# Kernel tuning notes

Hardware: AMD Instinct MI355X
Metric: run time of the kernel (lower is better)

## Reference

```python
import jax, jax.numpy as jnp
import numpy as np
from jax import lax

MAXHD = 200.0
MAXV = 40.0
MINA = -6.0
MAXA = 4.0
DT = 0.1
PAST = 25
NVEH = 4096
NT = 256


def setup_inputs() -> dict:
    key = jax.random.key(0)
    ks = jax.random.split(key, 8)
    s = 0.1
    return dict(
        lead_states=jax.random.uniform(ks[0], (NVEH, NT + PAST - 1, 2), dtype=jnp.float32),
        cur_states=jax.random.uniform(ks[1], (NVEH, PAST, 2), dtype=jnp.float32),
        mask=jnp.ones((NVEH, NT + PAST - 1), dtype=jnp.float32),
        conv1_w=jax.random.normal(ks[2], (3, 3, 32), dtype=jnp.float32) * s,
        conv1_b=jnp.zeros((32,), dtype=jnp.float32),
        conv2_w=jax.random.normal(ks[3], (3, 32, 64), dtype=jnp.float32) * s,
        conv2_b=jnp.zeros((64,), dtype=jnp.float32),
        dense2_w=jax.random.normal(ks[4], (384, 10), dtype=jnp.float32) * s,
        dense2_b=jnp.zeros((10,), dtype=jnp.float32),
        dense1_w=jax.random.normal(ks[5], (10, 1), dtype=jnp.float32) * s,
        dense1_b=jnp.zeros((1,), dtype=jnp.float32),
        nt=NT,
    )


def reference(lead_states, cur_states, mask, conv1_w, conv1_b, conv2_w, conv2_b,
              dense2_w, dense2_b, dense1_w, dense1_b, nt):
    nveh = lead_states.shape[0]
    lead_pos = lead_states[:, :, 0]      # (nveh, nt+past-1)
    lead_speeds = lead_states[:, :, 1]

    dn = ('NWC', 'WIO', 'NWC')

    def cnn(x):
        # x: (nveh, PAST, 3)
        x = jax.nn.relu(lax.conv_general_dilated(x, conv1_w, (1,), 'SAME', dimension_numbers=dn) + conv1_b)
        x = lax.reduce_window(x, -jnp.inf, lax.max, (1, 2, 1), (1, 2, 1), 'SAME')   # (nveh,13,32)
        x = jax.nn.relu(lax.conv_general_dilated(x, conv2_w, (1,), 'VALID', dimension_numbers=dn) + conv2_b)
        x = lax.reduce_window(x, -jnp.inf, lax.max, (1, 2, 1), (1, 2, 1), 'SAME')   # (nveh,6,64)
        x = x.reshape(x.shape[0], -1)                                               # (nveh,384)
        x = jax.nn.relu(x @ dense2_w + dense2_b)
        x = x @ dense1_w + dense1_b                                                 # (nveh,1)
        return (MAXA - MINA) * x + MINA

    def step(carry, t):
        cur_pos, cur_speeds = carry                    # each (nveh, PAST)
        lp = lax.dynamic_slice(lead_pos, (0, t), (nveh, PAST))
        ls = lax.dynamic_slice(lead_speeds, (0, t), (nveh, PAST))
        x = jnp.stack([(lp - cur_pos) / MAXHD, cur_speeds / MAXV, ls / MAXV], axis=2)
        acc = cnn(x)                                   # (nveh,1)
        pred_pos = cur_pos[:, -1:] + DT * cur_speeds[:, -1:]
        pred_sp = cur_speeds[:, -1:] + DT * acc
        new_pos = jnp.concatenate([cur_pos[:, 1:], pred_pos], axis=1)
        new_sp = jnp.concatenate([cur_speeds[:, 1:], pred_sp], axis=1)
        return (new_pos, new_sp), (pred_pos[:, 0], pred_sp[:, 0])

    init = (cur_states[:, :, 0], cur_states[:, :, 1])
    _, (pos_preds, speed_preds) = lax.scan(step, init, jnp.arange(nt))
    # (nt, nveh) -> (nveh, nt, 2)
    return jnp.stack([pos_preds.T, speed_preds.T], axis=2)
```

## Files before the change

### kernel.cpp

```cpp
#include <hip/hip_runtime.h>
#include <stdint.h>


#define PAST 25
#define NTW_MAX 280

typedef __attribute__((ext_vector_type(8))) short bf16x8;
typedef __attribute__((ext_vector_type(4))) float f32x4;
typedef unsigned short u16x2 __attribute__((ext_vector_type(2)));
#define MFMA16 __builtin_amdgcn_mfma_f32_16x16x32_bf16

static __device__ __forceinline__ uint32_t f2bf(float f) {
  union { float f; uint32_t u; } x; x.f = f;
  return (x.u + 0x7FFFu + ((x.u >> 16) & 1u)) >> 16;
}
static __device__ __forceinline__ float bf2f(uint32_t b) {
  union { uint32_t u; float f; } x; x.u = b << 16; return x.f;
}
static __device__ __forceinline__ uint32_t pkbf(float lo, float hi) {
  uint32_t r;
  asm("v_cvt_pk_bf16_f32 %0, %1, %2" : "=v"(r) : "v"(lo), "v"(hi));
  return r;
}
static __device__ __forceinline__ f32x4 bcast4(float v) { f32x4 r = {v, v, v, v}; return r; }

static __device__ __forceinline__ uint32_t pkmax(uint32_t a, uint32_t b) {
#if __has_builtin(__builtin_elementwise_max)
  union U { uint32_t w; u16x2 v; } x, y; x.w = a; y.w = b;
  x.v = __builtin_elementwise_max(x.v, y.v);
  return x.w;
#else
  uint32_t al = a << 16, bl = b << 16;
  uint32_t lo = (al > bl ? al : bl) >> 16;
  uint32_t ah = a & 0xffff0000u, bh = b & 0xffff0000u;
  uint32_t hi = ah > bh ? ah : bh;
  return lo | hi;
#endif
}
static __device__ __forceinline__ uint4 maxq(uint4 a, uint4 b) {
  uint4 r; r.x = pkmax(a.x, b.x); r.y = pkmax(a.y, b.y);
  r.z = pkmax(a.z, b.z); r.w = pkmax(a.w, b.w); return r;
}
static __device__ __forceinline__ int w21(int x) { if (x >= 21) x -= 21; if (x >= 21) x -= 21; return x; }
static __device__ __forceinline__ int w17(int x) { if (x >= 17) x -= 17; if (x >= 17) x -= 17; return x; }
static __device__ __forceinline__ void lds_fence() {
  asm volatile("s_waitcnt lgkmcnt(0)" ::: "memory");
}
static __device__ __forceinline__ float rsum16(float x) {
  x += __builtin_bit_cast(float, __builtin_amdgcn_update_dpp(0, __builtin_bit_cast(int, x), 0x121, 0xf, 0xf, true));
  x += __builtin_bit_cast(float, __builtin_amdgcn_update_dpp(0, __builtin_bit_cast(int, x), 0x122, 0xf, 0xf, true));
  x += __builtin_bit_cast(float, __builtin_amdgcn_update_dpp(0, __builtin_bit_cast(int, x), 0x124, 0xf, 0xf, true));
  x += __builtin_bit_cast(float, __builtin_amdgcn_update_dpp(0, __builtin_bit_cast(int, x), 0x128, 0xf, 0xf, true));
  return x;
}

union FragU { bf16x8 v; uint16_t u[8]; uint4 q; };
struct RowD { f32x4 d0, d1; };

struct __align__(16) SMem {
  uint32_t Xcol[8][33][2];
  float2 lead[8][NTW_MAX];
  uint16_t P[24 * 8 * 32];
  uint16_t O2[20 * 8 * 64];
  float2 obuf[2][8][64];
  f32x4 JpartA[2][64];
  f32x4 JpartB[2][64];
};

__global__ __launch_bounds__(256, 2) void rnncf_kernel(
    const float* __restrict__ lead_states, const float* __restrict__ cur_states,
    const float* __restrict__ conv1_w, const float* __restrict__ conv1_b,
    const float* __restrict__ conv2_w, const float* __restrict__ conv2_b,
    const float* __restrict__ dense2_w, const float* __restrict__ dense2_b,
    const float* __restrict__ dense1_w, const float* __restrict__ dense1_b,
    float* __restrict__ out, int nt, int ntw) {
  __shared__ SMem sm;
  const int tid = threadIdx.x;
  const int lane = tid & 63;
  const int wid = tid >> 6;
  const int n = lane & 15;
  const int quad = lane >> 4;
  const int vbase = blockIdx.x * 8;

  if (tid < 200) {
    int v = tid & 7, u = tid >> 3;
    const float2 l = *(const float2*)(lead_states + ((size_t)(vbase + v) * ntw + u) * 2);
    const float2 c = *(const float2*)(cur_states + ((size_t)(vbase + v) * PAST + u) * 2);
    float x0 = (l.x - c.x) * 0.005f;
    uint32_t w0 = pkbf(x0, c.y * 0.025f);
    sm.Xcol[v][u][0] = w0;
    sm.Xcol[v][u][1] = pkbf(l.y * 0.025f, x0 - bf2f(w0 & 0xffffu));
  }
#pragma unroll
  for (int v = 0; v < 8; ++v)
    for (int i = tid; i < ntw; i += 256)
      sm.lead[v][i] = *(const float2*)(lead_states + ((size_t)(vbase + v) * ntw + i) * 2);

  float pos_s = 0.f, spd_s = 0.f;
  if (wid == 3 && quad < 2 && n < 4) {
    int veh = quad * 4 + n;
    const float2 c = *(const float2*)(cur_states + ((size_t)(vbase + veh) * PAST + 24) * 2);
    pos_s = c.x * 0.005f; spd_s = c.y * 0.025f;
  }

  FragU B1[2];
#pragma unroll
  for (int ct = 0; ct < 2; ++ct)
#pragma unroll
    for (int jj = 0; jj < 8; ++jj) {
      int k = quad * 8 + jj;
      int dw = k & 3, cig = (k >> 2) & 3;
      float w = 0.f;
      if (k < 16 && dw < 3) {
        int ci = (cig == 3) ? 0 : cig;
        w = conv1_w[(dw * 3 + ci) * 32 + ct * 16 + n];
      }
      B1[ct].u[jj] = (uint16_t)f2bf(w);
    }
  FragU B2[3][4];
#pragma unroll
  for (int dw = 0; dw < 3; ++dw)
#pragma unroll
    for (int ct = 0; ct < 4; ++ct)
#pragma unroll
      for (int jj = 0; jj < 8; ++jj) {
        int kap = quad * 8 + jj;
        int ci = (kap & 1) * 16 + (kap >> 1);
        B2[dw][ct].u[jj] = (uint16_t)f2bf(conv2_w[(dw * 32 + ci) * 64 + ct * 16 + n]);
      }
  FragU Bd[12];
#pragma unroll
  for (int kt = 0; kt < 12; ++kt)
#pragma unroll
    for (int jj = 0; jj < 8; ++jj) {
      int flat = kt * 32 + quad * 8 + jj;
      int jp = flat >> 6, kap = flat & 63;
      int co = (kap & 3) * 16 + (kap >> 2);
      Bd[kt].u[jj] = (uint16_t)f2bf((n < 10) ? dense2_w[(jp * 64 + co) * 10 + n] : 0.f);
    }
  const float b1v0 = conv1_b[n], b1v1 = conv1_b[16 + n];
  float b2v[4];
#pragma unroll
  for (int ct = 0; ct < 4; ++ct) b2v[ct] = conv2_b[ct * 16 + n];
  const float d2bv = (n < 10) ? dense2_b[n] : 0.f;
  const float wd1v = (n < 10) ? dense1_w[n] : 0.f;
  const float bd1v = dense1_b[0];

  auto pIdx = [&](int s, int veh, int ch) { return ((s * 8 + veh) * 4 + ch) * 8; };
  auto oIdx = [&](int s, int veh, int ch) { return ((s * 8 + veh) * 8 + ch) * 8; };

  auto build_x = [&](int c, int padL, int padR) -> FragU {
    int h = quad & 1, v8 = n & 7;
    uint32_t d0 = padL ? 0u : sm.Xcol[v8][(c - 1) & 31][h];
    uint32_t d1 = sm.Xcol[v8][c & 31][h];
    uint32_t d2 = padR ? 0u : sm.Xcol[v8][(c + 1) & 31][h];
    FragU a;
    a.q.x = __builtin_amdgcn_perm(d1, d0, 0x05040100u);
    a.q.y = d2 & 0xffffu;
    a.q.z = __builtin_amdgcn_perm(d1, d0, 0x07060302u);
    a.q.w = d2 >> 16;
    return a;
  };

  auto conv1_row = [&](int c, int padL, int padR) -> RowD {
    FragU a = build_x(c, padL, padR);
    RowD rd;
    rd.d0 = MFMA16(a.v, B1[0].v, bcast4(b1v0), 0, 0, 0);
    rd.d1 = MFMA16(a.v, B1[1].v, bcast4(b1v1), 0, 0, 0);
    return rd;
  };

  auto pool_write = [&](const RowD& A, const RowD& Bq, int ds) {
    if (quad < 2) {
#pragma unroll
      for (int r = 0; r < 4; ++r) {
        float e0 = fmaxf(fmaxf(A.d0[r], Bq.d0[r]), 0.f);
        float e1 = fmaxf(fmaxf(A.d1[r], Bq.d1[r]), 0.f);
        int veh = quad * 4 + r;
        *(uint32_t*)&sm.P[pIdx(ds, veh, (n >> 2) ^ (veh & 3)) + (n & 3) * 2] = pkbf(e0, e1);
      }
    }
  };

  auto pool_write1 = [&](const RowD& A, int ds) {
    if (quad < 2) {
#pragma unroll
      for (int r = 0; r < 4; ++r) {
        float e0 = fmaxf(A.d0[r], 0.f), e1 = fmaxf(A.d1[r], 0.f);
        int veh = quad * 4 + r;
        *(uint32_t*)&sm.P[pIdx(ds, veh, (n >> 2) ^ (veh & 3)) + (n & 3) * 2] = pkbf(e0, e1);
      }
    }
  };

  auto ld_P = [&](int s) -> FragU {
    FragU a; a.q = *(const uint4*)&sm.P[pIdx(s, n & 7, quad ^ (n & 3))]; return a;
  };

  auto conv2_acc = [&](f32x4* acc, int slot, int dw) {
    FragU a = ld_P(slot);
#pragma unroll
    for (int ct = 0; ct < 4; ++ct) acc[ct] = MFMA16(a.v, B2[dw][ct].v, acc[ct], 0, 0, 0);
  };

  auto conv2_accf = [&](f32x4* acc, const FragU& a, int dw) {
#pragma unroll
    for (int ct = 0; ct < 4; ++ct) acc[ct] = MFMA16(a.v, B2[dw][ct].v, acc[ct], 0, 0, 0);
  };

  auto o2_write = [&](const f32x4* acc, int ds) {
    if (quad < 2) {
#pragma unroll
      for (int r = 0; r < 4; ++r) {
        int veh = quad * 4 + r;
        float m0 = fmaxf(acc[0][r], 0.f), m1 = fmaxf(acc[1][r], 0.f);
        float m2 = fmaxf(acc[2][r], 0.f), m3 = fmaxf(acc[3][r], 0.f);
        uint2 w2; w2.x = pkbf(m0, m1); w2.y = pkbf(m2, m3);
        *(uint2*)&sm.O2[oIdx(ds, veh, (n >> 1) ^ (veh & 7)) + (n & 1) * 4] = w2;
      }
    }
  };

  auto dense_jp = [&](int pa, int pb, int jp, f32x4& a0, f32x4& a1) {
#pragma unroll
    for (int hf = 0; hf < 2; ++hf) {
      uint4 qa = *(const uint4*)&sm.O2[oIdx(pa, n & 7, (hf * 4 + quad) ^ (n & 7))];
      if (pb >= 0) {
        uint4 qb = *(const uint4*)&sm.O2[oIdx(pb, n & 7, (hf * 4 + quad) ^ (n & 7))];
        qa = maxq(qa, qb);
      }
      FragU a; a.q = qa;
      if (hf == 0) a0 = MFMA16(a.v, Bd[jp * 2].v, a0, 0, 0, 0);
      else         a1 = MFMA16(a.v, Bd[jp * 2 + 1].v, a1, 0, 0, 0);
    }
  };

  auto dense_jp_pre = [&](int pa, const uint4* qpre, int jp, f32x4& a0, f32x4& a1) {
#pragma unroll
    for (int hf = 0; hf < 2; ++hf) {
      uint4 qa = *(const uint4*)&sm.O2[oIdx(pa, n & 7, (hf * 4 + quad) ^ (n & 7))];
      if (qpre) qa = maxq(qa, qpre[hf]);
      FragU a; a.q = qa;
      if (hf == 0) a0 = MFMA16(a.v, Bd[jp * 2].v, a0, 0, 0, 0);
      else         a1 = MFMA16(a.v, Bd[jp * 2 + 1].v, a1, 0, 0, 0);
    }
  };

  auto flush_out = [&](int bi, int t0, int cnt) {
    int vv = lane >> 3;
    int s0 = (lane & 7) * 8;
#pragma unroll
    for (int k = 0; k < 8; ++k) {
      int s = s0 + k;
      if (s < cnt) {
        float2 d = sm.obuf[bi][vv][s];
        *(float2*)(out + ((size_t)(vbase + vv) * nt + t0 + s) * 2) = d;
      }
    }
  };

  __syncthreads();

#pragma unroll
  for (int i = 0; i < 5; ++i) {
    int g = 2 + wid + 4 * i;
    RowD A = conv1_row(g, 0, 0);
    RowD Bq = conv1_row(g + 1, 0, 0);
    pool_write(A, Bq, g % 21);
  }
  __syncthreads();

#pragma unroll
  for (int i = 0; i < 4; ++i) {
    int a = 2 + wid + 4 * i;
    f32x4 acc[4];
#pragma unroll
    for (int ct = 0; ct < 4; ++ct) acc[ct] = bcast4(b2v[ct]);
    conv2_acc(acc, a % 21, 0);
    conv2_acc(acc, (a + 2) % 21, 1);
    conv2_acc(acc, (a + 4) % 21, 2);
    o2_write(acc, a % 17);
  }
  __syncthreads();

  RowD c1A = {};
  f32x4 accA[4] = {}, accB[4] = {};
  if (wid == 1) {
    RowD A = conv1_row(0, 1, 0), Bq = conv1_row(1, 0, 0);
    pool_write(A, Bq, 23);
    lds_fence();
    f32x4 aj[4];
#pragma unroll
    for (int ct = 0; ct < 4; ++ct) aj[ct] = bcast4(b2v[ct]);
    conv2_acc(aj, 23, 0); conv2_acc(aj, 2, 1); conv2_acc(aj, 4, 2);
    o2_write(aj, 17);
  } else if (wid == 2) {
    RowD A = conv1_row(1, 1, 0), Bq = conv1_row(2, 0, 0);
    pool_write(A, Bq, 1);
    lds_fence();
    f32x4 aj[4];
#pragma unroll
    for (int ct = 0; ct < 4; ++ct) aj[ct] = bcast4(b2v[ct]);
    conv2_acc(aj, 1, 0); conv2_acc(aj, 3, 1); conv2_acc(aj, 5, 2);
    o2_write(aj, 18);
  } else if (wid == 0) {
    RowD A = conv1_row(2, 1, 0), Bq = conv1_row(3, 0, 0);
    pool_write(A, Bq, 21);
  } else {
#pragma unroll
    for (int ct = 0; ct < 4; ++ct) accA[ct] = bcast4(b2v[ct]);
    conv2_acc(accA, 18, 0);
    conv2_acc(accA, 20, 1);
#pragma unroll
    for (int ct = 0; ct < 4; ++ct) accB[ct] = bcast4(b2v[ct]);
    conv2_acc(accB, 20, 0);
    c1A = conv1_row(22, 0, 0);
  }
  __syncthreads();

  if (wid == 0) {
    f32x4 a0 = bcast4(d2bv), a1 = bcast4(0.f);
    dense_jp(17, 2, 0, a0, a1);
    dense_jp(4, 6, 1, a0, a1);
    dense_jp(8, 10, 2, a0, a1);
    dense_jp(12, 14, 3, a0, a1);
    sm.JpartA[0][lane] = a0;
    sm.JpartB[0][lane] = a1;
  }
  __syncthreads();

  int tm21 = 0, tm17 = 0;
  for (int t = 0; t < nt; ++t) {
    const int sP22 = w21(tm21 + 22);
    const int sO16 = w17(tm17 + 16), sO18 = w17(tm17 + 18);
    const int tm21n = (tm21 + 1 == 21) ? 0 : tm21 + 1;
    const int tm17n = (tm17 + 1 == 17) ? 0 : tm17 + 1;
    const int sP18n = w21(tm21n + 18), sP20n = w21(tm21n + 20);

    if (wid == 3) {
      f32x4 jpA = sm.JpartA[t & 1][lane];
      f32x4 jpB = sm.JpartB[t & 1][lane];
      uint4 qj8[2];
#pragma unroll
      for (int hf = 0; hf < 2; ++hf)
        qj8[hf] = *(const uint4*)&sm.O2[oIdx(sO16, n & 7, (hf * 4 + quad) ^ (n & 7))];
      FragU fA18 = ld_P(sP18n);
      FragU fA20 = ld_P(sP20n);
      RowD Bq = conv1_row(t + 23, 0, 0);
      RowD Sg = conv1_row(t + 24, 0, 1);
      pool_write(c1A, Bq, sP22);
      pool_write1(Sg, 22);
      c1A = Bq;
      lds_fence();
      conv2_acc(accA, sP22, 2);
      conv2_acc(accB, sP22, 1);
      conv2_acc(accB, 22, 2);
      o2_write(accA, sO18);
      o2_write(accB, 19);
      lds_fence();
      f32x4 acc2 = bcast4(0.f), acc3 = bcast4(0.f);
      f32x4 acc4 = bcast4(0.f), acc5 = bcast4(0.f);
      dense_jp_pre(sO18, qj8, 4, acc2, acc3);
      dense_jp_pre(19, (const uint4*)nullptr, 5, acc4, acc5);
      float s0 = fmaxf(jpA[0] + jpB[0] + acc2[0] + acc3[0] + acc4[0] + acc5[0], 0.f) * wd1v;
      float s1 = fmaxf(jpA[1] + jpB[1] + acc2[1] + acc3[1] + acc4[1] + acc5[1], 0.f) * wd1v;
      float s2 = fmaxf(jpA[2] + jpB[2] + acc2[2] + acc3[2] + acc4[2] + acc5[2], 0.f) * wd1v;
      float s3 = fmaxf(jpA[3] + jpB[3] + acc2[3] + acc3[3] + acc4[3] + acc5[3], 0.f) * wd1v;
      s0 = rsum16(s0); s1 = rsum16(s1); s2 = rsum16(s2); s3 = rsum16(s3);
      if (quad < 2 && n < 4) {
        int veh = quad * 4 + n;
        float sv = (n == 0) ? s0 : (n == 1) ? s1 : (n == 2) ? s2 : s3;
        float accv = 10.f * (sv + bd1v) - 6.f;
        float np_s = pos_s + 0.02f * spd_s;
        float nsp = spd_s * 40.f + 0.1f * accv;
        pos_s = np_s; spd_s = nsp * 0.025f;
        float2 o2v; o2v.x = np_s * 200.f; o2v.y = nsp;
        sm.obuf[(t >> 6) & 1][veh][t & 63] = o2v;
        int ui = t + PAST; if (ui > ntw - 1) ui = ntw - 1;
        float2 ln = sm.lead[veh][ui];
        float x0 = ln.x * 0.005f - np_s;
        uint32_t wlo = pkbf(x0, spd_s);
        sm.Xcol[veh][(t + PAST) & 31][0] = wlo;
        sm.Xcol[veh][(t + PAST) & 31][1] = pkbf(ln.y * 0.025f, x0 - bf2f(wlo & 0xffffu));
      }
#pragma unroll
      for (int ct = 0; ct < 4; ++ct) accA[ct] = bcast4(b2v[ct]);
      conv2_accf(accA, fA18, 0);
      conv2_accf(accA, fA20, 1);
#pragma unroll
      for (int ct = 0; ct < 4; ++ct) accB[ct] = bcast4(b2v[ct]);
      conv2_accf(accB, fA20, 0);
    } else if (wid == 0) {
      f32x4 a0 = bcast4(d2bv), a1 = bcast4(0.f);
      dense_jp(17 + ((t + 1) & 1), w17(tm17n + 2), 0, a0, a1);
      dense_jp(w17(tm17n + 4), w17(tm17n + 6), 1, a0, a1);
      dense_jp(w17(tm17n + 8), w17(tm17n + 10), 2, a0, a1);
      dense_jp(w17(tm17n + 12), w17(tm17n + 14), 3, a0, a1);
      sm.JpartA[(t + 1) & 1][lane] = a0;
      sm.JpartB[(t + 1) & 1][lane] = a1;
    } else if (wid == 1) {
      if ((t & 63) == 0 && t > 0) flush_out(((t >> 6) & 1) ^ 1, t - 64, 64);
      f32x4 aj[4];
#pragma unroll
      for (int ct = 0; ct < 4; ++ct) aj[ct] = bcast4(b2v[ct]);
      conv2_acc(aj, (t & 1) ? 23 : 21, 0);
      conv2_acc(aj, w21(tm21 + 4), 1);
      conv2_acc(aj, w21(tm21 + 6), 2);
      o2_write(aj, 17 + (t & 1));
    } else {
      RowD A = conv1_row(t + 3, 1, 0);
      RowD Bq = conv1_row(t + 4, 0, 0);
      pool_write(A, Bq, (t & 1) ? 21 : 23);
    }
    __syncthreads();

    tm21 = tm21n; tm17 = tm17n;
  }

  if (wid == 1) {
    int t0 = (nt - 1) & ~63;
    flush_out(((nt - 1) >> 6) & 1, t0, nt - t0);
  }
}

extern "C" void kernel_launch(void* const* d_in, const int* in_sizes, int n_in,
                              void* d_out, int out_size, void* d_ws, size_t ws_size,
                              hipStream_t stream) {
  const float* lead = (const float*)d_in[0];
  const float* cur  = (const float*)d_in[1];
  const float* c1w = (const float*)d_in[3];
  const float* c1b = (const float*)d_in[4];
  const float* c2w = (const float*)d_in[5];
  const float* c2b = (const float*)d_in[6];
  const float* d2w = (const float*)d_in[7];
  const float* d2b = (const float*)d_in[8];
  const float* d1w = (const float*)d_in[9];
  const float* d1b = (const float*)d_in[10];
  float* out = (float*)d_out;

  int nveh = in_sizes[1] / (PAST * 2);
  int ntw  = in_sizes[2] / nveh;
  int nt   = ntw - PAST + 1;
  int nblocks = nveh / 8;

  rnncf_kernel<<<nblocks, 256, 0, stream>>>(lead, cur, c1w, c1b, c2w, c2b,
                                            d2w, d2b, d1w, d1b, out, nt, ntw);
}
```

Before: 436.6 us.

## Transpose conv1 MFMA, forward pooled fragments via bpermute, rotate wave roles per block

Conv1 now runs as a swapped-operand MFMA (weights as A, inputs as B), so each lane holds all four pooled values for one vehicle. These are packed into a single 128-bit LDS store instead of four scattered 32-bit stores. On the critical wave the pooled rows go straight into the conv2 operands through ds_bpermute, which removes an LDS round trip and a fence. The lead-state load and the partial-sum add are hoisted earlier, and wave roles are rotated by block index so the serial critical role lands on different SIMDs. The cost is extra bpermute traffic and more complex role indexing.

```diff
diff --git a/kernel.cpp b/kernel.cpp
--- a/kernel.cpp
+++ b/kernel.cpp
@@ -81,6 +81,8 @@
   const int n = lane & 15;
   const int quad = lane >> 4;
   const int vbase = blockIdx.x * 8;
+  const int role = (wid + (int)((blockIdx.x ^ (blockIdx.x >> 8)) & 3)) & 3;
+  const int bpidx = ((lane >> 4) << 6) | ((lane & 7) << 2);
 
   if (tid < 200) {
     int v = tid & 7, u = tid >> 3;
@@ -97,7 +99,7 @@
       sm.lead[v][i] = *(const float2*)(lead_states + ((size_t)(vbase + v) * ntw + i) * 2);
 
   float pos_s = 0.f, spd_s = 0.f;
-  if (wid == 3 && quad < 2 && n < 4) {
+  if (role == 3 && quad < 2 && n < 4) {
     int veh = quad * 4 + n;
     const float2 c = *(const float2*)(cur_states + ((size_t)(vbase + veh) * PAST + 24) * 2);
     pos_s = c.x * 0.005f; spd_s = c.y * 0.025f;
@@ -138,7 +140,12 @@
       int co = (kap & 3) * 16 + (kap >> 2);
       Bd[kt].u[jj] = (uint16_t)f2bf((n < 10) ? dense2_w[(jp * 64 + co) * 10 + n] : 0.f);
     }
-  const float b1v0 = conv1_b[n], b1v1 = conv1_b[16 + n];
+  f32x4 b1q0, b1q1;
+#pragma unroll
+  for (int r = 0; r < 4; ++r) {
+    b1q0[r] = conv1_b[quad * 4 + r];
+    b1q1[r] = conv1_b[16 + quad * 4 + r];
+  }
   float b2v[4];
 #pragma unroll
   for (int ct = 0; ct < 4; ++ct) b2v[ct] = conv2_b[ct * 16 + n];
@@ -162,35 +169,45 @@
     return a;
   };
 
-  auto conv1_row = [&](int c, int padL, int padR) -> RowD {
+  auto conv1s_row = [&](int c, int padL, int padR) -> RowD {
     FragU a = build_x(c, padL, padR);
     RowD rd;
-    rd.d0 = MFMA16(a.v, B1[0].v, bcast4(b1v0), 0, 0, 0);
-    rd.d1 = MFMA16(a.v, B1[1].v, bcast4(b1v1), 0, 0, 0);
+    rd.d0 = MFMA16(B1[0].v, a.v, b1q0, 0, 0, 0);
+    rd.d1 = MFMA16(B1[1].v, a.v, b1q1, 0, 0, 0);
     return rd;
   };
 
-  auto pool_write = [&](const RowD& A, const RowD& Bq, int ds) {
-    if (quad < 2) {
-#pragma unroll
-      for (int r = 0; r < 4; ++r) {
-        float e0 = fmaxf(fmaxf(A.d0[r], Bq.d0[r]), 0.f);
-        float e1 = fmaxf(fmaxf(A.d1[r], Bq.d1[r]), 0.f);
-        int veh = quad * 4 + r;
-        *(uint32_t*)&sm.P[pIdx(ds, veh, (n >> 2) ^ (veh & 3)) + (n & 3) * 2] = pkbf(e0, e1);
-      }
-    }
-  };
-
-  auto pool_write1 = [&](const RowD& A, int ds) {
-    if (quad < 2) {
-#pragma unroll
-      for (int r = 0; r < 4; ++r) {
-        float e0 = fmaxf(A.d0[r], 0.f), e1 = fmaxf(A.d1[r], 0.f);
-        int veh = quad * 4 + r;
-        *(uint32_t*)&sm.P[pIdx(ds, veh, (n >> 2) ^ (veh & 3)) + (n & 3) * 2] = pkbf(e0, e1);
-      }
-    }
+  auto relumax4 = [&](const f32x4& a, const f32x4& b) -> f32x4 {
+    f32x4 r;
+#pragma unroll
+    for (int i = 0; i < 4; ++i) r[i] = fmaxf(fmaxf(a[i], b[i]), 0.f);
+    return r;
+  };
+  auto relu4 = [&](const f32x4& a) -> f32x4 {
+    f32x4 r;
+#pragma unroll
+    for (int i = 0; i < 4; ++i) r[i] = fmaxf(a[i], 0.f);
+    return r;
+  };
+  auto pack4 = [&](const f32x4& p0, const f32x4& p1) -> uint4 {
+    uint4 w;
+    w.x = pkbf(p0[0], p1[0]); w.y = pkbf(p0[1], p1[1]);
+    w.z = pkbf(p0[2], p1[2]); w.w = pkbf(p0[3], p1[3]);
+    return w;
+  };
+  auto p_store = [&](const uint4& w, int ds) {
+    if (n < 8) *(uint4*)&sm.P[pIdx(ds, n, quad ^ (n & 3))] = w;
+  };
+  auto pool_store = [&](const RowD& A, const RowD& Bq, int ds) {
+    p_store(pack4(relumax4(A.d0, Bq.d0), relumax4(A.d1, Bq.d1)), ds);
+  };
+  auto bperm_frag = [&](const uint4& w) -> FragU {
+    FragU f;
+    f.q.x = (uint32_t)__builtin_amdgcn_ds_bpermute(bpidx, (int)w.x);
+    f.q.y = (uint32_t)__builtin_amdgcn_ds_bpermute(bpidx, (int)w.y);
+    f.q.z = (uint32_t)__builtin_amdgcn_ds_bpermute(bpidx, (int)w.z);
+    f.q.w = (uint32_t)__builtin_amdgcn_ds_bpermute(bpidx, (int)w.w);
+    return f;
   };
 
   auto ld_P = [&](int s) -> FragU {
@@ -264,9 +281,9 @@
 #pragma unroll
   for (int i = 0; i < 5; ++i) {
     int g = 2 + wid + 4 * i;
-    RowD A = conv1_row(g, 0, 0);
-    RowD Bq = conv1_row(g + 1, 0, 0);
-    pool_write(A, Bq, g % 21);
+    RowD A = conv1s_row(g, 0, 0);
+    RowD Bq = conv1s_row(g + 1, 0, 0);
+    pool_store(A, Bq, g % 21);
   }
   __syncthreads();
 
@@ -285,27 +302,27 @@
 
   RowD c1A = {};
   f32x4 accA[4] = {}, accB[4] = {};
-  if (wid == 1) {
-    RowD A = conv1_row(0, 1, 0), Bq = conv1_row(1, 0, 0);
-    pool_write(A, Bq, 23);
+  if (role == 1) {
+    RowD A = conv1s_row(0, 1, 0), Bq = conv1s_row(1, 0, 0);
+    pool_store(A, Bq, 23);
     lds_fence();
     f32x4 aj[4];
 #pragma unroll
     for (int ct = 0; ct < 4; ++ct) aj[ct] = bcast4(b2v[ct]);
     conv2_acc(aj, 23, 0); conv2_acc(aj, 2, 1); conv2_acc(aj, 4, 2);
     o2_write(aj, 17);
-  } else if (wid == 2) {
-    RowD A = conv1_row(1, 1, 0), Bq = conv1_row(2, 0, 0);
-    pool_write(A, Bq, 1);
+  } else if (role == 2) {
+    RowD A = conv1s_row(1, 1, 0), Bq = conv1s_row(2, 0, 0);
+    pool_store(A, Bq, 1);
     lds_fence();
     f32x4 aj[4];
 #pragma unroll
     for (int ct = 0; ct < 4; ++ct) aj[ct] = bcast4(b2v[ct]);
     conv2_acc(aj, 1, 0); conv2_acc(aj, 3, 1); conv2_acc(aj, 5, 2);
     o2_write(aj, 18);
-  } else if (wid == 0) {
-    RowD A = conv1_row(2, 1, 0), Bq = conv1_row(3, 0, 0);
-    pool_write(A, Bq, 21);
+  } else if (role == 0) {
+    RowD A = conv1s_row(2, 1, 0), Bq = conv1s_row(3, 0, 0);
+    pool_store(A, Bq, 21);
   } else {
 #pragma unroll
     for (int ct = 0; ct < 4; ++ct) accA[ct] = bcast4(b2v[ct]);
@@ -314,11 +331,11 @@
 #pragma unroll
     for (int ct = 0; ct < 4; ++ct) accB[ct] = bcast4(b2v[ct]);
     conv2_acc(accB, 20, 0);
-    c1A = conv1_row(22, 0, 0);
+    c1A = conv1s_row(22, 0, 0);
   }
   __syncthreads();
 
-  if (wid == 0) {
+  if (role == 0) {
     f32x4 a0 = bcast4(d2bv), a1 = bcast4(0.f);
     dense_jp(17, 2, 0, a0, a1);
     dense_jp(4, 6, 1, a0, a1);
@@ -337,7 +354,7 @@
     const int tm17n = (tm17 + 1 == 17) ? 0 : tm17 + 1;
     const int sP18n = w21(tm21n + 18), sP20n = w21(tm21n + 20);
 
-    if (wid == 3) {
+    if (role == 3) {
       f32x4 jpA = sm.JpartA[t & 1][lane];
       f32x4 jpB = sm.JpartB[t & 1][lane];
       uint4 qj8[2];
@@ -346,15 +363,21 @@
         qj8[hf] = *(const uint4*)&sm.O2[oIdx(sO16, n & 7, (hf * 4 + quad) ^ (n & 7))];
       FragU fA18 = ld_P(sP18n);
       FragU fA20 = ld_P(sP20n);
-      RowD Bq = conv1_row(t + 23, 0, 0);
-      RowD Sg = conv1_row(t + 24, 0, 1);
-      pool_write(c1A, Bq, sP22);
-      pool_write1(Sg, 22);
+      float2 ln = {0.f, 0.f};
+      int ui = t + PAST; if (ui > ntw - 1) ui = ntw - 1;
+      if (quad < 2 && n < 4) ln = sm.lead[quad * 4 + n][ui];
+      f32x4 jpS = jpA + jpB;
+      RowD Bq = conv1s_row(t + 23, 0, 0);
+      RowD Sg = conv1s_row(t + 24, 0, 1);
+      uint4 w11 = pack4(relumax4(c1A.d0, Bq.d0), relumax4(c1A.d1, Bq.d1));
+      uint4 w12 = pack4(relu4(Sg.d0), relu4(Sg.d1));
+      p_store(w11, sP22);
       c1A = Bq;
-      lds_fence();
-      conv2_acc(accA, sP22, 2);
-      conv2_acc(accB, sP22, 1);
-      conv2_acc(accB, 22, 2);
+      FragU f11 = bperm_frag(w11);
+      FragU f12 = bperm_frag(w12);
+      conv2_accf(accA, f11, 2);
+      conv2_accf(accB, f11, 1);
+      conv2_accf(accB, f12, 2);
       o2_write(accA, sO18);
       o2_write(accB, 19);
       lds_fence();
@@ -362,10 +385,10 @@
       f32x4 acc4 = bcast4(0.f), acc5 = bcast4(0.f);
       dense_jp_pre(sO18, qj8, 4, acc2, acc3);
       dense_jp_pre(19, (const uint4*)nullptr, 5, acc4, acc5);
-      float s0 = fmaxf(jpA[0] + jpB[0] + acc2[0] + acc3[0] + acc4[0] + acc5[0], 0.f) * wd1v;
-      float s1 = fmaxf(jpA[1] + jpB[1] + acc2[1] + acc3[1] + acc4[1] + acc5[1], 0.f) * wd1v;
-      float s2 = fmaxf(jpA[2] + jpB[2] + acc2[2] + acc3[2] + acc4[2] + acc5[2], 0.f) * wd1v;
-      float s3 = fmaxf(jpA[3] + jpB[3] + acc2[3] + acc3[3] + acc4[3] + acc5[3], 0.f) * wd1v;
+      float s0 = fmaxf(jpS[0] + acc2[0] + acc3[0] + acc4[0] + acc5[0], 0.f) * wd1v;
+      float s1 = fmaxf(jpS[1] + acc2[1] + acc3[1] + acc4[1] + acc5[1], 0.f) * wd1v;
+      float s2 = fmaxf(jpS[2] + acc2[2] + acc3[2] + acc4[2] + acc5[2], 0.f) * wd1v;
+      float s3 = fmaxf(jpS[3] + acc2[3] + acc3[3] + acc4[3] + acc5[3], 0.f) * wd1v;
       s0 = rsum16(s0); s1 = rsum16(s1); s2 = rsum16(s2); s3 = rsum16(s3);
       if (quad < 2 && n < 4) {
         int veh = quad * 4 + n;
@@ -376,8 +399,6 @@
         pos_s = np_s; spd_s = nsp * 0.025f;
         float2 o2v; o2v.x = np_s * 200.f; o2v.y = nsp;
         sm.obuf[(t >> 6) & 1][veh][t & 63] = o2v;
-        int ui = t + PAST; if (ui > ntw - 1) ui = ntw - 1;
-        float2 ln = sm.lead[veh][ui];
         float x0 = ln.x * 0.005f - np_s;
         uint32_t wlo = pkbf(x0, spd_s);
         sm.Xcol[veh][(t + PAST) & 31][0] = wlo;
@@ -390,7 +411,7 @@
 #pragma unroll
       for (int ct = 0; ct < 4; ++ct) accB[ct] = bcast4(b2v[ct]);
       conv2_accf(accB, fA20, 0);
-    } else if (wid == 0) {
+    } else if (role == 0) {
       f32x4 a0 = bcast4(d2bv), a1 = bcast4(0.f);
       dense_jp(17 + ((t + 1) & 1), w17(tm17n + 2), 0, a0, a1);
       dense_jp(w17(tm17n + 4), w17(tm17n + 6), 1, a0, a1);
@@ -398,7 +419,7 @@
       dense_jp(w17(tm17n + 12), w17(tm17n + 14), 3, a0, a1);
       sm.JpartA[(t + 1) & 1][lane] = a0;
       sm.JpartB[(t + 1) & 1][lane] = a1;
-    } else if (wid == 1) {
+    } else if (role == 1) {
       if ((t & 63) == 0 && t > 0) flush_out(((t >> 6) & 1) ^ 1, t - 64, 64);
       f32x4 aj[4];
 #pragma unroll
@@ -408,16 +429,16 @@
       conv2_acc(aj, w21(tm21 + 6), 2);
       o2_write(aj, 17 + (t & 1));
     } else {
-      RowD A = conv1_row(t + 3, 1, 0);
-      RowD Bq = conv1_row(t + 4, 0, 0);
-      pool_write(A, Bq, (t & 1) ? 21 : 23);
+      RowD A = conv1s_row(t + 3, 1, 0);
+      RowD Bq = conv1s_row(t + 4, 0, 0);
+      pool_store(A, Bq, (t & 1) ? 21 : 23);
     }
     __syncthreads();
 
     tm21 = tm21n; tm17 = tm17n;
   }
 
-  if (wid == 1) {
+  if (role == 1) {
     int t0 = (nt - 1) & ~63;
     flush_out(((nt - 1) >> 6) & 1, t0, nt - t0);
   }
```

Result: slower. 477.2 us (+9.3%).
